# Optimization experiments

Measured on AMD Instinct MI355X. Metric: run time of the kernel, lower is better.

## Reference

```python
import jax, jax.numpy as jnp
import numpy as np

D_MODEL = 1024
N_HEADS = 16
D_K = D_MODEL // N_HEADS
NEG_INF = -1.0e9


def setup_inputs() -> dict:
    key = jax.random.key(0)
    ks = jax.random.split(key, 12)
    B, S = 2, 2048
    inp = {
        "q": jax.random.normal(ks[0], (B, S, D_MODEL), dtype=jnp.float32),
        "k": jax.random.normal(ks[1], (B, S, D_MODEL), dtype=jnp.float32),
        "v": jax.random.normal(ks[2], (B, S, D_MODEL), dtype=jnp.float32),
        "mask": jax.random.randint(ks[3], (B, 1, S, S), 0, 2, dtype=jnp.int32),
        "Wq": jax.random.normal(ks[4], (D_MODEL, D_MODEL), dtype=jnp.float32) / np.sqrt(D_MODEL),
        "bq": jnp.zeros((D_MODEL,), dtype=jnp.float32),
        "Wk": jax.random.normal(ks[5], (D_MODEL, D_MODEL), dtype=jnp.float32) / np.sqrt(D_MODEL),
        "bk": jnp.zeros((D_MODEL,), dtype=jnp.float32),
        "Wv": jax.random.normal(ks[6], (D_MODEL, D_MODEL), dtype=jnp.float32) / np.sqrt(D_MODEL),
        "bv": jnp.zeros((D_MODEL,), dtype=jnp.float32),
        "Wo": jax.random.normal(ks[7], (D_MODEL, D_MODEL), dtype=jnp.float32) / np.sqrt(D_MODEL),
        "bo": jnp.zeros((D_MODEL,), dtype=jnp.float32),
    }
    return inp


def _split_heads(x):
    B, S, _ = x.shape
    return x.reshape(B, S, N_HEADS, D_K).transpose(0, 2, 1, 3)  # [B,H,S,Dk]


def reference(q, k, v, mask, Wq, bq, Wk, bk, Wv, bv, Wo, bo):
    # QKV projections (nn.Linear: x @ W.T + b; here W stored as [in,out]-agnostic square)
    query = _split_heads(q @ Wq + bq)
    key_ = _split_heads(k @ Wk + bk)
    value = _split_heads(v @ Wv + bv)

    scale = 1.0 / np.sqrt(D_K).astype(np.float32)
    scores = jnp.einsum("bhqd,bhkd->bhqk", query, key_) * scale  # [B,H,S,S]
    scores = jnp.where(mask == 0, NEG_INF, scores)
    attn = jax.nn.softmax(scores, axis=-1)  # dropout is identity in eval (p=0.0)
    ctx = jnp.einsum("bhqk,bhkd->bhqd", attn, value)  # [B,H,S,Dk]

    B, H, S, Dk = ctx.shape
    ctx = ctx.transpose(0, 2, 1, 3).reshape(B, S, H * Dk)
    return ctx @ Wo + bo
```

## Files before the change

### kernel.cpp

```cpp
#include <hip/hip_runtime.h>
#include <hip/hip_bf16.h>

typedef __bf16 bf16_t;
typedef __bf16 bf16x2 __attribute__((ext_vector_type(2)));
typedef __bf16 bf16x8 __attribute__((ext_vector_type(8)));
typedef float f32x4 __attribute__((ext_vector_type(4)));
typedef float f32x16 __attribute__((ext_vector_type(16)));
typedef int intx4 __attribute__((ext_vector_type(4)));
typedef unsigned int u32;
typedef unsigned long long u64;

#define S_LEN 2048
#define DM 1024
#define NH 16
#define DK 64
#define M_ROWS 4096
#define SCALE_LOG2E 0.1803368801111204f

__device__ __forceinline__ int sw_off(int row, int col) {
  return row * 64 + ((((col >> 3) ^ row) & 7) << 3) + (col & 7);
}

__device__ __forceinline__ bf16x8 cvt8(const float4& a, const float4& b) {
  bf16x8 v;
  v[0] = (__bf16)a.x; v[1] = (__bf16)a.y; v[2] = (__bf16)a.z; v[3] = (__bf16)a.w;
  v[4] = (__bf16)b.x; v[5] = (__bf16)b.y; v[6] = (__bf16)b.z; v[7] = (__bf16)b.w;
  return v;
}

__device__ __forceinline__ void glds16(const bf16_t* g, bf16_t* l) {
  __builtin_amdgcn_global_load_lds(
      (const __attribute__((address_space(1))) void*)g,
      (__attribute__((address_space(3))) void*)l, 16, 0, 0);
}

__device__ __forceinline__ int pk2(float lo, float hi) {
  bf16x2 t;
  t[0] = (__bf16)lo;
  t[1] = (__bf16)hi;
  return __builtin_bit_cast(int, t);
}

__global__ __launch_bounds__(256) void pack_mask(
    const int* __restrict__ mask, u64* __restrict__ mb)
{
  const int wgl = blockIdx.x * 4 + (threadIdx.x >> 6);
  const int lane = threadIdx.x & 63;
  const int q = wgl & 2047;
  const int kw = (wgl >> 11) & 31;
  const int b = wgl >> 16;
  const int val = mask[((size_t)(b * S_LEN + q)) * S_LEN + kw * 64 + lane];
  const u64 bits = __ballot(val != 0);
  if (lane == 0) mb[wgl] = bits;
}

__global__ __launch_bounds__(256) void cvt_inputs(
    const float* __restrict__ q, const float* __restrict__ k,
    const float* __restrict__ v, bf16_t* __restrict__ Xb)
{
  const int z = blockIdx.y;
  const float* __restrict__ src = (z == 0) ? q : ((z == 1) ? k : v);
  const size_t idx = ((size_t)blockIdx.x * 256 + threadIdx.x) * 8;
  const float4 a = *(const float4*)&src[idx];
  const float4 b = *(const float4*)&src[idx + 4];
  *(bf16x8*)&Xb[(size_t)z * M_ROWS * DM + idx] = cvt8(a, b);
}

__global__ __launch_bounds__(256) void transw_kernel(
    const float* __restrict__ Wq, const float* __restrict__ Wk,
    const float* __restrict__ Wv, const float* __restrict__ Wo,
    bf16_t* __restrict__ Wt)
{
  const int z = blockIdx.z;
  const float* __restrict__ W = (z == 0) ? Wq : ((z == 1) ? Wk : ((z == 2) ? Wv : Wo));
  bf16_t* __restrict__ out = Wt + (size_t)z * DM * DM;
  __shared__ float tile[64][65];
  const int tx = threadIdx.x & 31, ty = threadIdx.x >> 5;
  const int k0 = blockIdx.x * 64, n0 = blockIdx.y * 64;
  #pragma unroll
  for (int j = 0; j < 8; ++j) {
    const float2 v = *(const float2*)&W[(size_t)(k0 + ty + 8 * j) * DM + n0 + tx * 2];
    tile[ty + 8 * j][tx * 2] = v.x;
    tile[ty + 8 * j][tx * 2 + 1] = v.y;
  }
  __syncthreads();
  #pragma unroll
  for (int j = 0; j < 8; ++j) {
    const int a = ty + 8 * j;
    bf16x2 p;
    p[0] = (__bf16)tile[tx * 2][a];
    p[1] = (__bf16)tile[tx * 2 + 1][a];
    *(bf16x2*)&out[(size_t)(n0 + a) * DM + k0 + tx * 2] = p;
  }
}

__device__ __forceinline__ void gemm128_body(
    const bf16_t* __restrict__ A, const bf16_t* __restrict__ Bt,
    const float* __restrict__ bias, const float scale,
    bf16_t* __restrict__ outb, float* __restrict__ outf)
{
  __shared__ __align__(16) bf16_t As[128 * 32];
  __shared__ __align__(16) bf16_t Bs[128 * 32];
  const int t = threadIdx.x, w = t >> 6, L = t & 63, quad = L >> 4, l16 = L & 15;
  const int m0 = blockIdx.x * 128, n0 = blockIdx.y * 128;
  const int mb = 64 * (w & 1), nb = 64 * (w >> 1);
  const int rowS = t >> 2, subS = (t & 3) * 8;

  f32x4 acc[4][4] = {};
  for (int k0 = 0; k0 < DM; k0 += 32) {
    __syncthreads();
    glds16(&A[(size_t)(m0 + rowS) * DM + k0 + subS],        &As[t * 8]);
    glds16(&A[(size_t)(m0 + 64 + rowS) * DM + k0 + subS],   &As[2048 + t * 8]);
    glds16(&Bt[(size_t)(n0 + rowS) * DM + k0 + subS],       &Bs[t * 8]);
    glds16(&Bt[(size_t)(n0 + 64 + rowS) * DM + k0 + subS],  &Bs[2048 + t * 8]);
    __syncthreads();
    bf16x8 af[4], bfr[4];
    #pragma unroll
    for (int mt = 0; mt < 4; ++mt)
      af[mt] = *(const bf16x8*)&As[(mb + 16 * mt + l16) * 32 + quad * 8];
    #pragma unroll
    for (int ct = 0; ct < 4; ++ct)
      bfr[ct] = *(const bf16x8*)&Bs[(nb + 16 * ct + l16) * 32 + quad * 8];
    #pragma unroll
    for (int mt = 0; mt < 4; ++mt)
      #pragma unroll
      for (int ct = 0; ct < 4; ++ct)
        acc[mt][ct] = __builtin_amdgcn_mfma_f32_16x16x32_bf16(af[mt], bfr[ct], acc[mt][ct], 0, 0, 0);
  }
  #pragma unroll
  for (int mt = 0; mt < 4; ++mt)
    #pragma unroll
    for (int ct = 0; ct < 4; ++ct)
      #pragma unroll
      for (int r = 0; r < 4; ++r) {
        const int row = m0 + mb + 16 * mt + quad * 4 + r;
        const int n = n0 + nb + 16 * ct + l16;
        const float val = (acc[mt][ct][r] + bias[n]) * scale;
        if (outb) outb[(size_t)row * DM + n] = (__bf16)val;
        else      outf[(size_t)row * DM + n] = val;
      }
}

__global__ __launch_bounds__(256) void gemm_qkv(
    const bf16_t* __restrict__ Xb, const bf16_t* __restrict__ Wt,
    const float* __restrict__ bq, const float* __restrict__ bk,
    const float* __restrict__ bv, bf16_t* __restrict__ QKVb)
{
  const int z = blockIdx.z;
  gemm128_body(Xb + (size_t)z * M_ROWS * DM, Wt + (size_t)z * DM * DM,
               (z == 0) ? bq : ((z == 1) ? bk : bv),
               (z == 0) ? SCALE_LOG2E : 1.0f,
               QKVb + (size_t)z * M_ROWS * DM, nullptr);
}

__global__ __launch_bounds__(256) void gemm_out(
    const bf16_t* __restrict__ ctx, const bf16_t* __restrict__ Wto,
    const float* __restrict__ bo, float* __restrict__ out)
{
  gemm128_body(ctx, Wto, bo, 1.0f, nullptr, out);
}

__global__ __launch_bounds__(256) void transpV(
    const bf16_t* __restrict__ Vb, bf16_t* __restrict__ Vtw)
{
  __shared__ bf16_t Tr[64 * 72];
  const int t = threadIdx.x;
  const int key0 = blockIdx.x * 64;
  const int bh = blockIdx.y, b = bh >> 4, h = bh & 15;
  const int r = t >> 2, c = (t & 3) * 16;
  const bf16_t* src = &Vb[(size_t)(b * S_LEN + key0 + r) * DM + h * DK + c];
  const bf16x8 v0 = *(const bf16x8*)src;
  const bf16x8 v1 = *(const bf16x8*)(src + 8);
  #pragma unroll
  for (int j = 0; j < 8; ++j) {
    Tr[r * 72 + c + j] = v0[j];
    Tr[r * 72 + c + 8 + j] = v1[j];
  }
  __syncthreads();
  const int dv = t >> 2, kc = (t & 3) * 16;
  bf16_t ov[16];
  #pragma unroll
  for (int j = 0; j < 16; ++j) ov[j] = Tr[(kc + j) * 72 + dv];
  bf16_t* dst = &Vtw[((size_t)bh * DK + dv) * S_LEN + key0 + kc];
  *(bf16x8*)dst = *(bf16x8*)&ov[0];
  *(bf16x8*)(dst + 8) = *(bf16x8*)&ov[8];
}

__global__ __launch_bounds__(256, 2) void attn_kernel(
    const bf16_t* __restrict__ Qb, const bf16_t* __restrict__ Kb,
    const bf16_t* __restrict__ Vtw, const u64* __restrict__ mb,
    bf16_t* __restrict__ ctx)
{
  __shared__ __align__(16) bf16_t KVs[2][2][64 * 64];

  const int t = threadIdx.x, w = t >> 6, L = t & 63;
  const int l31 = L & 31, h5 = L >> 5;
  const int q0 = blockIdx.x * 128;
  const int bh = blockIdx.y, b = bh >> 4, h = bh & 15;

  bf16x8 qf[4];
  {
    const bf16_t* qsrc =
        &Qb[(size_t)(b * S_LEN + q0 + 32 * w + l31) * DM + h * DK + 8 * h5];
    #pragma unroll
    for (int ks = 0; ks < 4; ++ks) qf[ks] = *(const bf16x8*)(qsrc + 16 * ks);
  }

  const int ch = (L & 7) ^ (L >> 3);
  const int row0 = 16 * w + (L >> 3);
  const int kofs0 = w * 1024 + L * 8, kofs1 = kofs0 + 512;
  const bf16_t* pK0 = &Kb[(size_t)(b * S_LEN + row0) * DM + h * DK + ch * 8];
  const bf16_t* pK1 = pK0 + (size_t)8 * DM;
  const bf16_t* pV0 = &Vtw[((size_t)bh * DK + row0) * S_LEN + ch * 8];
  const bf16_t* pV1 = pV0 + (size_t)8 * S_LEN;

  const u64* pm = &mb[(size_t)b * 32 * S_LEN + q0 + 32 * w + l31];

  auto stageKV = [&](int buf) {
    glds16(pK0, &KVs[buf][0][kofs0]);
    glds16(pK1, &KVs[buf][0][kofs1]);
    glds16(pV0, &KVs[buf][1][kofs0]);
    glds16(pV1, &KVs[buf][1][kofs1]);
    pK0 += (size_t)64 * DM; pK1 += (size_t)64 * DM;
    pV0 += 64; pV1 += 64;
  };

  f32x16 O[2] = {};
  float l_lane = 0.f;

  auto compute = [&](int buf, u64 mcur) {
    const bf16_t* __restrict__ Kc = &KVs[buf][0][0];
    const bf16_t* __restrict__ Vc = &KVs[buf][1][0];
    f32x16 s0 = {}, s1 = {};
    __builtin_amdgcn_s_setprio(1);
    #pragma unroll
    for (int ks = 0; ks < 4; ++ks) {
      const bf16x8 kf0 = *(const bf16x8*)&Kc[sw_off(l31, ks * 16 + 8 * h5)];
      const bf16x8 kf1 = *(const bf16x8*)&Kc[sw_off(32 + l31, ks * 16 + 8 * h5)];
      s0 = __builtin_amdgcn_mfma_f32_32x32x16_bf16(kf0, qf[ks], s0, 0, 0, 0);
      s1 = __builtin_amdgcn_mfma_f32_32x32x16_bf16(kf1, qf[ks], s1, 0, 0, 0);
    }
    __builtin_amdgcn_s_setprio(0);
    #pragma unroll
    for (int nt = 0; nt < 2; ++nt) {
      const u32 mm = ((u32)(mcur >> (nt ? 32 : 0))) >> (4 * h5);
      const f32x16 sacc = nt ? s1 : s0;
      float p[16];
      #pragma unroll
      for (int r = 0; r < 16; ++r) {
        const int cb = (r & 3) + 8 * (r >> 2);
        const u32 mr = (u32)(((int)(mm << (31 - cb))) >> 31);
        const float e = __builtin_exp2f(sacc[r]);
        const float pv = __builtin_bit_cast(float, __builtin_bit_cast(u32, e) & mr);
        l_lane += pv;
        p[r] = pv;
      }
      #pragma unroll
      for (int ss = 0; ss < 2; ++ss) {
        const int x0 = pk2(p[8 * ss + 0], p[8 * ss + 1]);
        const int x1 = pk2(p[8 * ss + 2], p[8 * ss + 3]);
        const int y0 = pk2(p[8 * ss + 4], p[8 * ss + 5]);
        const int y1 = pk2(p[8 * ss + 6], p[8 * ss + 7]);
        const auto r0 = __builtin_amdgcn_permlane32_swap(x0, y0, false, false);
        const auto r1 = __builtin_amdgcn_permlane32_swap(x1, y1, false, false);
        intx4 wv;
        wv[0] = r0[0]; wv[1] = r1[0]; wv[2] = r0[1]; wv[3] = r1[1];
        const bf16x8 pf = __builtin_bit_cast(bf16x8, wv);
        const int s4 = 2 * nt + ss;
        const bf16x8 vf0 = *(const bf16x8*)&Vc[sw_off(l31, s4 * 16 + 8 * h5)];
        const bf16x8 vf1 = *(const bf16x8*)&Vc[sw_off(32 + l31, s4 * 16 + 8 * h5)];
        __builtin_amdgcn_s_setprio(1);
        O[0] = __builtin_amdgcn_mfma_f32_32x32x16_bf16(vf0, pf, O[0], 0, 0, 0);
        O[1] = __builtin_amdgcn_mfma_f32_32x32x16_bf16(vf1, pf, O[1], 0, 0, 0);
        __builtin_amdgcn_s_setprio(0);
      }
    }
  };

  stageKV(0);
  u64 mcur = *pm; pm += S_LEN;
  u64 mnext;
  __syncthreads();

  for (int kt = 0; kt < S_LEN / 64; kt += 2) {
    stageKV(1);
    mnext = *pm; pm += S_LEN;
    compute(0, mcur);
    __syncthreads();
    mcur = mnext;
    if (kt + 2 < S_LEN / 64) {
      stageKV(0);
      mnext = *pm; pm += S_LEN;
    }
    compute(1, mcur);
    __syncthreads();
    mcur = mnext;
  }

  const float lsum = l_lane + __shfl_xor(l_lane, 32);
  const float inv = 1.f / lsum;
  bf16_t* sc = &KVs[0][0][0] + (size_t)w * 2048;
  #pragma unroll
  for (int ot = 0; ot < 2; ++ot)
    #pragma unroll
    for (int r = 0; r < 16; ++r) {
      const int dv = 32 * ot + (r & 3) + 8 * (r >> 2) + 4 * h5;
      sc[sw_off(l31, dv)] = (__bf16)(O[ot][r] * inv);
    }
  const int erow = L >> 1, ecol = (L & 1) * 32;
  bf16_t* dst = &ctx[(size_t)(b * S_LEN + q0 + 32 * w + erow) * DM + h * DK + ecol];
  #pragma unroll
  for (int c8 = 0; c8 < 4; ++c8)
    *(bf16x8*)(dst + 8 * c8) = *(const bf16x8*)&sc[sw_off(erow, ecol + 8 * c8)];
}

extern "C" void kernel_launch(void* const* d_in, const int* in_sizes, int n_in,
                              void* d_out, int out_size, void* d_ws, size_t ws_size,
                              hipStream_t stream) {
  const float* q  = (const float*)d_in[0];
  const float* k  = (const float*)d_in[1];
  const float* v  = (const float*)d_in[2];
  const int* mask = (const int*)d_in[3];
  const float* Wq = (const float*)d_in[4];
  const float* bq = (const float*)d_in[5];
  const float* Wk = (const float*)d_in[6];
  const float* bk = (const float*)d_in[7];
  const float* Wv = (const float*)d_in[8];
  const float* bv = (const float*)d_in[9];
  const float* Wo = (const float*)d_in[10];
  const float* bo = (const float*)d_in[11];
  float* out = (float*)d_out;

  const size_t SLICE = (size_t)M_ROWS * DM;
  bf16_t* Xb   = (bf16_t*)d_ws;
  bf16_t* QKVb = Xb + 3 * SLICE;
  bf16_t* Wt   = QKVb + 3 * SLICE;
  u64* mbw     = (u64*)(Wt + (size_t)4 * DM * DM);
  bf16_t* ctx  = Xb;
  bf16_t* Vtw  = Xb + SLICE;

  pack_mask<<<dim3(32768), dim3(256), 0, stream>>>(mask, mbw);
  cvt_inputs<<<dim3(2048, 3), dim3(256), 0, stream>>>(q, k, v, Xb);
  transw_kernel<<<dim3(16, 16, 4), dim3(256), 0, stream>>>(Wq, Wk, Wv, Wo, Wt);
  gemm_qkv<<<dim3(32, 8, 3), dim3(256), 0, stream>>>(Xb, Wt, bq, bk, bv, QKVb);
  transpV<<<dim3(32, 32), dim3(256), 0, stream>>>(QKVb + 2 * SLICE, Vtw);
  attn_kernel<<<dim3(16, 32), dim3(256), 0, stream>>>(QKVb, QKVb + SLICE, Vtw, mbw, ctx);
  gemm_out<<<dim3(32, 8), dim3(256), 0, stream>>>(ctx, Wt + (size_t)3 * DM * DM, bo, out);
}
```

Before: 280.2 us.

## Restructure attention into 512-thread blocks with XCD-aware mapping and register-staged KV prefetch

The attention kernel now uses 512-thread blocks covering 256 query rows and a 1D grid of 256 blocks. Each block index is remapped so that blocks sharing the same batch-head land on the same XCD, improving L2 reuse of K/V. Async global-to-LDS copies are replaced by register prefetch of 128 keys per iteration, written to LDS after compute, which halves the number of barriers per key. The setprio hints are removed. In exchange it uses more LDS and registers per block and exposes load latency through register staging, and only 256 blocks are launched.

```diff
diff --git a/kernel.cpp b/kernel.cpp
--- a/kernel.cpp
+++ b/kernel.cpp
@@ -186,53 +186,41 @@
   *(bf16x8*)(dst + 8) = *(bf16x8*)&ov[8];
 }
 
-__global__ __launch_bounds__(256, 2) void attn_kernel(
+__global__ __launch_bounds__(512, 2) void attn_kernel(
     const bf16_t* __restrict__ Qb, const bf16_t* __restrict__ Kb,
     const bf16_t* __restrict__ Vtw, const u64* __restrict__ mb,
     bf16_t* __restrict__ ctx)
 {
-  __shared__ __align__(16) bf16_t KVs[2][2][64 * 64];
+  __shared__ __align__(16) bf16_t KVs[2][4][64 * 64];
 
   const int t = threadIdx.x, w = t >> 6, L = t & 63;
   const int l31 = L & 31, h5 = L >> 5;
-  const int q0 = blockIdx.x * 128;
-  const int bh = blockIdx.y, b = bh >> 4, h = bh & 15;
-
+  const int g = blockIdx.x;
+  const int xcd = g & 7, slot = g >> 3;
+  const int bh = xcd * 4 + (slot >> 3), qt = slot & 7;
+  const int q0 = qt * 256;
+  const int b = bh >> 4, h = bh & 15;
+
+  const int qr = q0 + 32 * w + l31;
   bf16x8 qf[4];
   {
-    const bf16_t* qsrc =
-        &Qb[(size_t)(b * S_LEN + q0 + 32 * w + l31) * DM + h * DK + 8 * h5];
+    const bf16_t* qsrc = &Qb[(size_t)(b * S_LEN + qr) * DM + h * DK + 8 * h5];
     #pragma unroll
     for (int ks = 0; ks < 4; ++ks) qf[ks] = *(const bf16x8*)(qsrc + 16 * ks);
   }
 
-  const int ch = (L & 7) ^ (L >> 3);
-  const int row0 = 16 * w + (L >> 3);
-  const int kofs0 = w * 1024 + L * 8, kofs1 = kofs0 + 512;
-  const bf16_t* pK0 = &Kb[(size_t)(b * S_LEN + row0) * DM + h * DK + ch * 8];
-  const bf16_t* pK1 = pK0 + (size_t)8 * DM;
-  const bf16_t* pV0 = &Vtw[((size_t)bh * DK + row0) * S_LEN + ch * 8];
-  const bf16_t* pV1 = pV0 + (size_t)8 * S_LEN;
-
-  const u64* pm = &mb[(size_t)b * 32 * S_LEN + q0 + 32 * w + l31];
-
-  auto stageKV = [&](int buf) {
-    glds16(pK0, &KVs[buf][0][kofs0]);
-    glds16(pK1, &KVs[buf][0][kofs1]);
-    glds16(pV0, &KVs[buf][1][kofs0]);
-    glds16(pV1, &KVs[buf][1][kofs1]);
-    pK0 += (size_t)64 * DM; pK1 += (size_t)64 * DM;
-    pV0 += 64; pV1 += 64;
-  };
+  const int rk = t >> 3;
+  const int ck = (t & 7) ^ (rk & 7);
+  const bf16_t* pK = &Kb[(size_t)(b * S_LEN + rk) * DM + h * DK + ck * 8];
+  const bf16_t* pV = &Vtw[((size_t)bh * DK + rk) * S_LEN + ck * 8];
+  const u64* pm = &mb[(size_t)b * 32 * S_LEN + qr];
 
   f32x16 O[2] = {};
   float l_lane = 0.f;
 
-  auto compute = [&](int buf, u64 mcur) {
-    const bf16_t* __restrict__ Kc = &KVs[buf][0][0];
-    const bf16_t* __restrict__ Vc = &KVs[buf][1][0];
+  auto compute = [&](const bf16_t* __restrict__ Kc, const bf16_t* __restrict__ Vc,
+                     u64 mcur) {
     f32x16 s0 = {}, s1 = {};
-    __builtin_amdgcn_s_setprio(1);
     #pragma unroll
     for (int ks = 0; ks < 4; ++ks) {
       const bf16x8 kf0 = *(const bf16x8*)&Kc[sw_off(l31, ks * 16 + 8 * h5)];
@@ -240,7 +228,6 @@
       s0 = __builtin_amdgcn_mfma_f32_32x32x16_bf16(kf0, qf[ks], s0, 0, 0, 0);
       s1 = __builtin_amdgcn_mfma_f32_32x32x16_bf16(kf1, qf[ks], s1, 0, 0, 0);
     }
-    __builtin_amdgcn_s_setprio(0);
     #pragma unroll
     for (int nt = 0; nt < 2; ++nt) {
       const u32 mm = ((u32)(mcur >> (nt ? 32 : 0))) >> (4 * h5);
@@ -269,32 +256,45 @@
         const int s4 = 2 * nt + ss;
         const bf16x8 vf0 = *(const bf16x8*)&Vc[sw_off(l31, s4 * 16 + 8 * h5)];
         const bf16x8 vf1 = *(const bf16x8*)&Vc[sw_off(32 + l31, s4 * 16 + 8 * h5)];
-        __builtin_amdgcn_s_setprio(1);
         O[0] = __builtin_amdgcn_mfma_f32_32x32x16_bf16(vf0, pf, O[0], 0, 0, 0);
         O[1] = __builtin_amdgcn_mfma_f32_32x32x16_bf16(vf1, pf, O[1], 0, 0, 0);
-        __builtin_amdgcn_s_setprio(0);
       }
     }
   };
 
-  stageKV(0);
-  u64 mcur = *pm; pm += S_LEN;
-  u64 mnext;
+  bf16x8 k0r = *(const bf16x8*)pK;
+  bf16x8 k1r = *(const bf16x8*)(pK + (size_t)64 * DM);
+  bf16x8 v0r = *(const bf16x8*)pV;
+  bf16x8 v1r = *(const bf16x8*)(pV + 64);
+  u64 m0 = pm[0], m1 = pm[S_LEN];
+  pK += (size_t)128 * DM; pV += 128; pm += 2 * S_LEN;
+  *(bf16x8*)&KVs[0][0][t * 8] = k0r;
+  *(bf16x8*)&KVs[0][1][t * 8] = k1r;
+  *(bf16x8*)&KVs[0][2][t * 8] = v0r;
+  *(bf16x8*)&KVs[0][3][t * 8] = v1r;
   __syncthreads();
 
-  for (int kt = 0; kt < S_LEN / 64; kt += 2) {
-    stageKV(1);
-    mnext = *pm; pm += S_LEN;
-    compute(0, mcur);
+  for (int kt = 0; kt < S_LEN / 128; ++kt) {
+    const int cur = kt & 1;
+    u64 n0 = 0, n1 = 0;
+    if (kt + 1 < S_LEN / 128) {
+      k0r = *(const bf16x8*)pK;
+      k1r = *(const bf16x8*)(pK + (size_t)64 * DM);
+      v0r = *(const bf16x8*)pV;
+      v1r = *(const bf16x8*)(pV + 64);
+      n0 = pm[0]; n1 = pm[S_LEN];
+      pK += (size_t)128 * DM; pV += 128; pm += 2 * S_LEN;
+    }
+    compute(&KVs[cur][0][0], &KVs[cur][2][0], m0);
+    compute(&KVs[cur][1][0], &KVs[cur][3][0], m1);
+    if (kt + 1 < S_LEN / 128) {
+      *(bf16x8*)&KVs[cur ^ 1][0][t * 8] = k0r;
+      *(bf16x8*)&KVs[cur ^ 1][1][t * 8] = k1r;
+      *(bf16x8*)&KVs[cur ^ 1][2][t * 8] = v0r;
+      *(bf16x8*)&KVs[cur ^ 1][3][t * 8] = v1r;
+      m0 = n0; m1 = n1;
+    }
     __syncthreads();
-    mcur = mnext;
-    if (kt + 2 < S_LEN / 64) {
-      stageKV(0);
-      mnext = *pm; pm += S_LEN;
-    }
-    compute(1, mcur);
-    __syncthreads();
-    mcur = mnext;
   }
 
   const float lsum = l_lane + __shfl_xor(l_lane, 32);
@@ -344,6 +344,6 @@
   transw_kernel<<<dim3(16, 16, 4), dim3(256), 0, stream>>>(Wq, Wk, Wv, Wo, Wt);
   gemm_qkv<<<dim3(32, 8, 3), dim3(256), 0, stream>>>(Xb, Wt, bq, bk, bv, QKVb);
   transpV<<<dim3(32, 32), dim3(256), 0, stream>>>(QKVb + 2 * SLICE, Vtw);
-  attn_kernel<<<dim3(16, 32), dim3(256), 0, stream>>>(QKVb, QKVb + SLICE, Vtw, mbw, ctx);
+  attn_kernel<<<dim3(256), dim3(512), 0, stream>>>(QKVb, QKVb + SLICE, Vtw, mbw, ctx);
   gemm_out<<<dim3(32, 8), dim3(256), 0, stream>>>(ctx, Wt + (size_t)3 * DM * DM, bo, out);
 }
```

New measurement: 287.4 us. +2.6%, slower.
